# Kernel tuning notes

Measured on AMD Instinct MI355X. Metric: run time of the kernel, lower is better.

Reference implementation:

```python
import jax, jax.numpy as jnp
import numpy as np

B = 512    # batch
C = 64     # total categorical columns (32 admission + 32 discharge)
N = 32     # graph nodes (one per clinical variable)
V = 100    # categories per column
EMB = 32   # entity embedding dim
HID = 64   # TGCN hidden channels
E = 256    # edges
T = 37     # periods (max LOS)


def setup_inputs() -> dict:
    key = jax.random.key(0)
    ks = jax.random.split(key, 16)

    def lin(k, fi, fo):
        return jax.random.normal(k, (fi, fo), jnp.float32) / np.float32(np.sqrt(fi))

    return {
        "x_batch": jax.random.randint(ks[0], (B, C), 0, V),
        "LOS_batch": jax.random.randint(ks[1], (B,), 0, 38).astype(jnp.int32),
        "template_edge_index": jax.random.randint(ks[2], (2, E), 0, N),
        # per-column entity embedding tables [C, V, EMB]
        "emb_table": jax.random.normal(ks[3], (C, V, EMB), jnp.float32) * 0.05,
        # TGCN gate GCN weights/biases
        "W_z": lin(ks[4], EMB, HID), "b_z": jnp.zeros((HID,), jnp.float32),
        "W_r": lin(ks[5], EMB, HID), "b_r": jnp.zeros((HID,), jnp.float32),
        "W_h": lin(ks[6], EMB, HID), "b_h": jnp.zeros((HID,), jnp.float32),
        # TGCN gate linear layers (input = concat(conv_out, H))
        "L_z": lin(ks[7], 2 * HID, HID), "lb_z": jnp.zeros((HID,), jnp.float32),
        "L_r": lin(ks[8], 2 * HID, HID), "lb_r": jnp.zeros((HID,), jnp.float32),
        "L_h": lin(ks[9], 2 * HID, HID), "lb_h": jnp.zeros((HID,), jnp.float32),
        # A3TGCN temporal attention parameter over periods
        "att": jax.random.uniform(ks[10], (T,), jnp.float32),
        # classifier MLP (num_classes=2 -> out_dim=1)
        "Wc1": lin(ks[11], HID, 2 * HID), "bc1": jnp.zeros((2 * HID,), jnp.float32),
        "Wc2": lin(ks[12], 2 * HID, 1), "bc2": jnp.zeros((1,), jnp.float32),
    }


def reference(x_batch, LOS_batch, template_edge_index, emb_table,
              W_z, b_z, W_r, b_r, W_h, b_h,
              L_z, lb_z, L_r, lb_r, L_h, lb_h,
              att, Wc1, bc1, Wc2, bc2):
    # --- entity embedding: one table per column -> [B, C, EMB]
    x_emb = emb_table[jnp.arange(C)[None, :], x_batch]
    ad, dis = x_emb[:, :N], x_emb[:, N:]              # [B, N, EMB] each

    # --- to_temporal: admission features while t < LOS, discharge after
    mask = jnp.arange(T)[None, None, None, :] < LOS_batch[:, None, None, None]
    x_temporal = jnp.where(mask, ad[..., None], dis[..., None])  # [B,N,EMB,T]

    # --- GCN symmetric normalization with self loops (PyG gcn_norm)
    loops = jnp.arange(N)
    src = jnp.concatenate([template_edge_index[0], loops])
    dst = jnp.concatenate([template_edge_index[1], loops])
    deg = jnp.zeros((N,), x_emb.dtype).at[dst].add(1.0)
    dinv = jnp.where(deg > 0, deg ** -0.5, 0.0)
    norm = dinv[src] * dinv[dst]                      # [E+N]

    def gcn(x, W, b):                                 # x: [B,N,Fin] -> [B,N,HID]
        xw = x @ W
        msg = xw[:, src, :] * norm[None, :, None]
        return jnp.zeros((B, N, W.shape[1]), x.dtype).at[:, dst, :].add(msg) + b

    H0 = jnp.zeros((B, N, HID), x_emb.dtype)          # hidden state (A3TGCN passes H=None each period)

    def tgcn_cell(Xt):                                # Xt: [B,N,EMB]
        Z = jax.nn.sigmoid(jnp.concatenate([gcn(Xt, W_z, b_z), H0], -1) @ L_z + lb_z)
        R = jax.nn.sigmoid(jnp.concatenate([gcn(Xt, W_r, b_r), H0], -1) @ L_r + lb_r)
        Ht = jnp.tanh(jnp.concatenate([gcn(Xt, W_h, b_h), H0 * R], -1) @ L_h + lb_h)
        return Z * H0 + (1.0 - Z) * Ht

    probs = jax.nn.softmax(att)
    Xs = jnp.moveaxis(x_temporal, -1, 0)              # [T,B,N,EMB]

    def step(acc, p_X):
        p, Xt = p_X
        return acc + p * tgcn_cell(Xt), None

    H_accum, _ = jax.lax.scan(step, H0, (probs, Xs))  # [B,N,HID]
    pooled = H_accum.mean(axis=1)                     # [B,HID]
    return jax.nn.relu(pooled @ Wc1 + bc1) @ Wc2 + bc2  # [B,1]
```

## Files before the change

### kernel.cpp

```cpp
#include <hip/hip_runtime.h>
#include <math.h>

#define BATCH 512
#define CCH   64
#define NND   32
#define VOC   100
#define DEMB  32
#define HID   64
#define NEDGE 256
#define NT    37

__device__ float gT[2 * CCH * VOC * HID];
__device__ float gA[NND * NND];
__device__ float gCB[2 * HID];
__device__ float gPC[NT + 1];

__global__ __launch_bounds__(512)
void a3_prep(const int* __restrict__ tei, const float* __restrict__ att,
             const float* __restrict__ emb,
             const float* __restrict__ Wz, const float* __restrict__ bz,
             const float* __restrict__ Wh, const float* __restrict__ bh,
             const float* __restrict__ Lz, const float* __restrict__ lbz,
             const float* __restrict__ Lh, const float* __restrict__ lbh) {
    __shared__ float sWL[2][DEMB][HID];
    __shared__ int   sdeg[NND];
    __shared__ float sdinv[NND];
    __shared__ float lA[NND][NND];

    const int tid = threadIdx.x;
    const int o   = tid & 63;
    const int wv  = tid >> 6;
    const int c   = blockIdx.x;

    {
        float az[4], ah[4];
#pragma unroll
        for (int i = 0; i < 4; ++i) { az[i] = 0.f; ah[i] = 0.f; }
        for (int m = 0; m < HID; ++m) {
            const float lz = Lz[m * HID + o];
            const float lh = Lh[m * HID + o];
#pragma unroll
            for (int i = 0; i < 4; ++i) {
                const int k = wv + 8 * i;
                az[i] = fmaf(Wz[k * HID + m], lz, az[i]);
                ah[i] = fmaf(Wh[k * HID + m], lh, ah[i]);
            }
        }
#pragma unroll
        for (int i = 0; i < 4; ++i) {
            sWL[0][wv + 8 * i][o] = az[i];
            sWL[1][wv + 8 * i][o] = ah[i];
        }
    }
    __syncthreads();

    for (int vi = 0; vi < 13; ++vi) {
        const int v = wv + 8 * vi;
        if (v < VOC) {
            float tz = 0.f, th = 0.f;
            for (int k = 0; k < DEMB; ++k) {
                const float e = emb[(c * VOC + v) * DEMB + k];
                tz = fmaf(e, sWL[0][k][o], tz);
                th = fmaf(e, sWL[1][k][o], th);
            }
            gT[((0 * CCH + c) * VOC + v) * HID + o] = tz;
            gT[((1 * CCH + c) * VOC + v) * HID + o] = th;
        }
    }

    if (blockIdx.x == 0) {
        if (tid < NND) sdeg[tid] = 1;
#pragma unroll
        for (int i = 0; i < 2; ++i) ((float*)lA)[tid + 512 * i] = 0.f;
        __syncthreads();
        int se = 0, de = 0;
        if (tid < NEDGE) {
            se = tei[tid]; de = tei[NEDGE + tid];
            atomicAdd(&sdeg[de], 1);
        }
        __syncthreads();
        if (tid < NND) sdinv[tid] = rsqrtf((float)sdeg[tid]);
        __syncthreads();
        if (tid < NEDGE) atomicAdd(&lA[de][se], sdinv[se] * sdinv[de]);
        if (tid < NND)   atomicAdd(&lA[tid][tid], sdinv[tid] * sdinv[tid]);
        __syncthreads();
#pragma unroll
        for (int i = 0; i < 2; ++i) gA[tid + 512 * i] = ((float*)lA)[tid + 512 * i];

        if (tid < 2 * HID) {
            const int g = tid >> 6, cc = tid & 63;
            const float* Lg  = g ? Lh  : Lz;
            const float* bg  = g ? bh  : bz;
            const float* lbg = g ? lbh : lbz;
            float s = lbg[cc];
            for (int k = 0; k < HID; ++k) s = fmaf(bg[k], Lg[k * HID + cc], s);
            gCB[tid] = s;
        }
        if (tid <= NT) {
            float m = att[0];
            for (int t = 1; t < NT; ++t) m = fmaxf(m, att[t]);
            float tot = 0.f, pre = 0.f;
            for (int t = 0; t < NT; ++t) {
                const float e = __expf(att[t] - m);
                tot += e;
                if (t < tid) pre += e;
            }
            gPC[tid] = pre / tot;
        }
    }
}

__global__ __launch_bounds__(512, 4)
void a3_main(const int* __restrict__ xbg, const int* __restrict__ LOSb,
             const float* __restrict__ Wc1, const float* __restrict__ bc1,
             const float* __restrict__ Wc2, const float* __restrict__ bc2,
             float* __restrict__ out) {
    __shared__ float sA[NND][NND];
    __shared__ int   srb[2][CCH];
    __shared__ float scb[2][HID];
    __shared__ float part[8][HID];
    __shared__ float pooled[HID];
    __shared__ float h1s[2 * HID];

    const int b   = blockIdx.x;
    const int tid = threadIdx.x;
    const int hd  = tid & 63;
    const int wv  = tid >> 6;

#pragma unroll
    for (int i = 0; i < 2; ++i) ((float*)sA)[tid + 512 * i] = gA[tid + 512 * i];
    if (tid < CCH) {
        const int xbv = xbg[b * CCH + tid];
        srb[0][tid] = ((0 * CCH + tid) * VOC + xbv) * HID;
        srb[1][tid] = ((1 * CCH + tid) * VOC + xbv) * HID;
    }
    if (tid < 2 * HID) ((float*)scb)[tid] = gCB[tid];
    const float cA = gPC[LOSb[b]];
    const float cD = 1.0f - cA;
    __syncthreads();

    const int var = wv >> 2;
    const int n0  = (wv & 3) * 8;
    float zacc[8], hacc[8];
#pragma unroll
    for (int j = 0; j < 8; ++j) { zacc[j] = 0.f; hacc[j] = 0.f; }
    for (int q = 0; q < NND; ++q) {
        const int cc = var * NND + q;
        const float tz = gT[srb[0][cc] + hd];
        const float th = gT[srb[1][cc] + hd];
#pragma unroll
        for (int j = 0; j < 8; ++j) {
            const float a = sA[n0 + j][q];
            zacc[j] = fmaf(a, tz, zacc[j]);
            hacc[j] = fmaf(a, th, hacc[j]);
        }
    }
    const float wr = var ? cD : cA;
    float psum = 0.f;
#pragma unroll
    for (int j = 0; j < 8; ++j) {
        const float zl = zacc[j] + scb[0][hd];
        const float hl = hacc[j] + scb[1][hd];
        const float Z  = 1.0f / (1.0f + __expf(-zl));
        const float e2 = __expf(2.0f * hl);
        const float Ht = (e2 - 1.0f) / (e2 + 1.0f);
        psum = fmaf(1.0f - Z, Ht, psum);
    }
    part[wv][hd] = wr * psum;
    __syncthreads();

    if (tid < HID) {
        float s = 0.f;
#pragma unroll
        for (int g = 0; g < 8; ++g) s += part[g][tid];
        pooled[tid] = s * (1.0f / NND);
    }
    __syncthreads();

    if (tid < 2 * HID) {
        float a = bc1[tid];
#pragma unroll 4
        for (int k = 0; k < HID; ++k) a = fmaf(pooled[k], Wc1[k * 2 * HID + tid], a);
        h1s[tid] = fmaxf(a, 0.f) * Wc2[tid];
    }
    __syncthreads();
    if (tid < 64) {
        float v = h1s[tid] + h1s[tid + 64];
#pragma unroll
        for (int off = 32; off; off >>= 1) v += __shfl_down(v, off);
        if (tid == 0) out[b] = v + bc2[0];
    }
}

extern "C" void kernel_launch(void* const* d_in, const int* in_sizes, int n_in,
                              void* d_out, int out_size, void* d_ws, size_t ws_size,
                              hipStream_t stream) {
    const int*   x_batch = (const int*)d_in[0];
    const int*   LOSb    = (const int*)d_in[1];
    const int*   tei     = (const int*)d_in[2];
    const float* emb     = (const float*)d_in[3];
    const float* Wz      = (const float*)d_in[4];
    const float* bz      = (const float*)d_in[5];
    const float* Wh      = (const float*)d_in[8];
    const float* bh      = (const float*)d_in[9];
    const float* Lz      = (const float*)d_in[10];
    const float* lbz     = (const float*)d_in[11];
    const float* Lh      = (const float*)d_in[14];
    const float* lbh     = (const float*)d_in[15];
    const float* att     = (const float*)d_in[16];
    const float* Wc1     = (const float*)d_in[17];
    const float* bc1     = (const float*)d_in[18];
    const float* Wc2     = (const float*)d_in[19];
    const float* bc2     = (const float*)d_in[20];
    float* outp = (float*)d_out;

    hipLaunchKernelGGL(a3_prep, dim3(CCH), dim3(512), 0, stream,
                       tei, att, emb, Wz, bz, Wh, bh, Lz, lbz, Lh, lbh);
    hipLaunchKernelGGL(a3_main, dim3(BATCH), dim3(512), 0, stream,
                       x_batch, LOSb, Wc1, bc1, Wc2, bc2, outp);
}
```

Before: 35.51 us.

## Split prep across more blocks, interleave z/h tables, fuse classifier tail

The prep kernel now launches four blocks per column, each producing a quarter of the vocabulary rows. This spreads the table build over more compute units, at the cost of each block recomputing the small W·L product. The z and h projection tables are stored interleaved as float2, so the main kernel does one 8-byte gather per column instead of two separate loads. Per-column row indices now come from a wave shuffle rather than a shared-memory offset table. The pooling and classifier MLP run in a single wave, which removes two block barriers.

Result: faster. 33.37 us (-6.0%).

```diff
diff --git a/kernel.cpp b/kernel.cpp
--- a/kernel.cpp
+++ b/kernel.cpp
@@ -10,10 +10,10 @@
 #define NEDGE 256
 #define NT    37
 
-__device__ float gT[2 * CCH * VOC * HID];
-__device__ float gA[NND * NND];
-__device__ float gCB[2 * HID];
-__device__ float gPC[NT + 1];
+__device__ float2 gT2[CCH * VOC * HID];
+__device__ float  gA[NND * NND];
+__device__ float  gCB[2 * HID];
+__device__ float  gPC[NT + 1];
 
 __global__ __launch_bounds__(512)
 void a3_prep(const int* __restrict__ tei, const float* __restrict__ att,
@@ -30,7 +30,8 @@
     const int tid = threadIdx.x;
     const int o   = tid & 63;
     const int wv  = tid >> 6;
-    const int c   = blockIdx.x;
+    const int c   = blockIdx.x >> 2;
+    const int vg  = blockIdx.x & 3;
 
     {
         float az[4], ah[4];
@@ -54,17 +55,18 @@
     }
     __syncthreads();
 
-    for (int vi = 0; vi < 13; ++vi) {
-        const int v = wv + 8 * vi;
-        if (v < VOC) {
+#pragma unroll
+    for (int vi = 0; vi < 4; ++vi) {
+        const int vl = wv + 8 * vi;
+        if (vl < 25) {
+            const int v = vg * 25 + vl;
             float tz = 0.f, th = 0.f;
             for (int k = 0; k < DEMB; ++k) {
                 const float e = emb[(c * VOC + v) * DEMB + k];
                 tz = fmaf(e, sWL[0][k][o], tz);
                 th = fmaf(e, sWL[1][k][o], th);
             }
-            gT[((0 * CCH + c) * VOC + v) * HID + o] = tz;
-            gT[((1 * CCH + c) * VOC + v) * HID + o] = th;
+            gT2[(c * VOC + v) * HID + o] = make_float2(tz, th);
         }
     }
 
@@ -116,46 +118,40 @@
              const float* __restrict__ Wc2, const float* __restrict__ bc2,
              float* __restrict__ out) {
     __shared__ float sA[NND][NND];
-    __shared__ int   srb[2][CCH];
     __shared__ float scb[2][HID];
     __shared__ float part[8][HID];
-    __shared__ float pooled[HID];
-    __shared__ float h1s[2 * HID];
-
-    const int b   = blockIdx.x;
-    const int tid = threadIdx.x;
-    const int hd  = tid & 63;
-    const int wv  = tid >> 6;
+    __shared__ float spool[HID];
+
+    const int b    = blockIdx.x;
+    const int tid  = threadIdx.x;
+    const int hd   = tid & 63;
+    const int wv   = tid >> 6;
+    const int var  = wv >> 2;
+    const int n0   = (wv & 3) * 8;
 
 #pragma unroll
     for (int i = 0; i < 2; ++i) ((float*)sA)[tid + 512 * i] = gA[tid + 512 * i];
-    if (tid < CCH) {
-        const int xbv = xbg[b * CCH + tid];
-        srb[0][tid] = ((0 * CCH + tid) * VOC + xbv) * HID;
-        srb[1][tid] = ((1 * CCH + tid) * VOC + xbv) * HID;
-    }
     if (tid < 2 * HID) ((float*)scb)[tid] = gCB[tid];
+    const int xv = xbg[b * CCH + var * NND + (tid & 31)];
     const float cA = gPC[LOSb[b]];
-    const float cD = 1.0f - cA;
     __syncthreads();
 
-    const int var = wv >> 2;
-    const int n0  = (wv & 3) * 8;
     float zacc[8], hacc[8];
 #pragma unroll
     for (int j = 0; j < 8; ++j) { zacc[j] = 0.f; hacc[j] = 0.f; }
+#pragma unroll 8
     for (int q = 0; q < NND; ++q) {
+        const int xq = __shfl(xv, q);
         const int cc = var * NND + q;
-        const float tz = gT[srb[0][cc] + hd];
-        const float th = gT[srb[1][cc] + hd];
+        const float2 t = gT2[(cc * VOC + xq) * HID + hd];
 #pragma unroll
         for (int j = 0; j < 8; ++j) {
             const float a = sA[n0 + j][q];
-            zacc[j] = fmaf(a, tz, zacc[j]);
-            hacc[j] = fmaf(a, th, hacc[j]);
-        }
-    }
-    const float wr = var ? cD : cA;
+            zacc[j] = fmaf(a, t.x, zacc[j]);
+            hacc[j] = fmaf(a, t.y, hacc[j]);
+        }
+    }
+    const float wr = var ? (1.0f - cA) : cA;
     float psum = 0.f;
 #pragma unroll
     for (int j = 0; j < 8; ++j) {
@@ -169,26 +165,22 @@
     part[wv][hd] = wr * psum;
     __syncthreads();
 
-    if (tid < HID) {
+    if (wv == 0) {
         float s = 0.f;
 #pragma unroll
-        for (int g = 0; g < 8; ++g) s += part[g][tid];
-        pooled[tid] = s * (1.0f / NND);
-    }
-    __syncthreads();
-
-    if (tid < 2 * HID) {
-        float a = bc1[tid];
-#pragma unroll 4
-        for (int k = 0; k < HID; ++k) a = fmaf(pooled[k], Wc1[k * 2 * HID + tid], a);
-        h1s[tid] = fmaxf(a, 0.f) * Wc2[tid];
-    }
-    __syncthreads();
-    if (tid < 64) {
-        float v = h1s[tid] + h1s[tid + 64];
+        for (int g = 0; g < 8; ++g) s += part[g][hd];
+        spool[hd] = s * (1.0f / NND);
+        float a0 = bc1[hd], a1 = bc1[hd + 64];
+#pragma unroll 8
+        for (int k = 0; k < HID; ++k) {
+            const float pk = spool[k];
+            a0 = fmaf(pk, Wc1[k * 2 * HID + hd], a0);
+            a1 = fmaf(pk, Wc1[k * 2 * HID + hd + 64], a1);
+        }
+        float v = fmaxf(a0, 0.f) * Wc2[hd] + fmaxf(a1, 0.f) * Wc2[hd + 64];
 #pragma unroll
         for (int off = 32; off; off >>= 1) v += __shfl_down(v, off);
-        if (tid == 0) out[b] = v + bc2[0];
+        if (hd == 0) out[b] = v + bc2[0];
     }
 }
 
@@ -214,7 +206,7 @@
     const float* bc2     = (const float*)d_in[20];
     float* outp = (float*)d_out;
 
-    hipLaunchKernelGGL(a3_prep, dim3(CCH), dim3(512), 0, stream,
+    hipLaunchKernelGGL(a3_prep, dim3(256), dim3(512), 0, stream,
                        tei, att, emb, Wz, bz, Wh, bh, Lz, lbz, Lh, lbh);
     hipLaunchKernelGGL(a3_main, dim3(BATCH), dim3(512), 0, stream,
                        x_batch, LOSb, Wc1, bc1, Wc2, bc2, outp);
```
